# Performance work log

Measured on AMD Instinct MI355X. Metric: run time of the kernel, lower is better.

The kernel has to match this reference:

```python
import jax, jax.numpy as jnp
import numpy as np

B, T, D = 64, 2048, 512
H = 64           # hidden_size
K, S = 3, 3      # kernel_size, stride
PAD = (K - 1) // 2
BATCH_FACTOR = 0.5


def _ceil_div(a, b):
    return -(-a // b)


def _conv1d(x, w, b, stride, padding):
    # x: [B, C_in, T], w: [C_out, C_in, K] (torch Conv1d layout), b: [C_out]
    y = jax.lax.conv_general_dilated(
        x, w, window_strides=(stride,), padding=[(padding, padding)],
        dimension_numbers=("NCH", "OIH", "NCH"))
    return y + b[None, :, None]


def _score_estimator(x, seq_lens, w1, b1, w2, b2):
    # x: [B, T, D] -> scores [B, T''], seq lens [B]
    xc = jnp.transpose(x, (0, 2, 1))                     # [B, D, T]
    h = _conv1d(xc, w1, b1, S, PAD)                      # [B, 2H, T']
    h = h.reshape(h.shape[0], H, 2, h.shape[-1]).max(axis=2)  # maxout pairs -> [B, H, T']
    s = _conv1d(h, w2, b2, S, PAD)[:, 0, :]              # [B, T'']
    sl = _ceil_div(seq_lens - K + 1 + 2 * PAD, S)
    sl = _ceil_div(sl - K + 1 + 2 * PAD, S)
    return s, sl


def setup_inputs() -> dict:
    key = jax.random.key(0)
    ks = jax.random.split(key, 6)
    x = jax.random.normal(ks[0], (B, T, D), dtype=jnp.float32)
    seq_lens = jax.random.randint(ks[1], (B,), T // 2, T + 1)
    w1 = jax.random.normal(ks[2], (2 * H, D, K), dtype=jnp.float32) * (1.0 / np.sqrt(D * K))
    b1 = jax.random.normal(ks[3], (2 * H,), dtype=jnp.float32) * 0.01
    w2 = jax.random.normal(ks[4], (1, H, K), dtype=jnp.float32) * (1.0 / np.sqrt(H * K))
    b2 = jax.random.normal(ks[5], (1,), dtype=jnp.float32) * 0.01
    return {"x": x, "seq_lens": seq_lens, "w1": w1, "b1": b1, "w2": w2, "b2": b2}


def reference(x, seq_lens, w1, b1, w2, b2):
    scores, scores_sl = _score_estimator(x, seq_lens, w1, b1, w2, b2)  # [B, T''], [B]
    # mean over (padded) time, rescaled by T''/seq_len (torch true division -> float)
    est = scores.mean(axis=1) * (scores.shape[1] / scores_sl.astype(jnp.float32))  # [B]
    k = int(scores.shape[0] * BATCH_FACTOR)
    _, idx = jax.lax.top_k(est, k)
    # torch builds a boolean mask + masked_select, which preserves original batch order
    idx = jnp.sort(idx)
    sel_lens = seq_lens[idx]                              # [B']
    x_sel = x[idx]                                        # [B', T, D]
    # torch also truncates time to max(sel_lens); drops only padding frames.
    # Done eagerly here (data-dependent shape, so not inside jit).
    max_time = int(jnp.max(sel_lens))
    x_sel = x_sel[:, :max_time, :]
    return x_sel, sel_lens
```

## Files before the change

kernel.cpp:

```cpp
#include <hip/hip_runtime.h>

#define T_LEN 2048
#define D_DIM 512
#define B_SZ  64
#define T1_LEN 683
#define NSEL  32
#define KTOT  1536
#define BK    64
#define TILE_T1 96
#define NTILES 8
#define NITER (KTOT / BK)

typedef __attribute__((ext_vector_type(8))) short bf16x8;
typedef __attribute__((ext_vector_type(4))) float f32x4;

constexpr size_t OFF_WHI = 0;
constexpr size_t OFF_WLO = 393216;
constexpr size_t OFF_EST = 786432;
constexpr size_t OFF_SEL = 786944;

__device__ inline unsigned bf16_rne(float x) {
    unsigned u = __float_as_uint(x);
    return (u + 0x7FFFu + ((u >> 16) & 1u)) >> 16;
}

__device__ inline unsigned bf16_rhu(float x) {
    return (__float_as_uint(x) + 0x8000u) >> 16;
}

__global__ __launch_bounds__(256) void pack_w1_split(const float* __restrict__ w1,
                                                     unsigned short* __restrict__ whi,
                                                     unsigned short* __restrict__ wlo,
                                                     float* __restrict__ est_raw) {
    if (blockIdx.x == 0 && threadIdx.x < 64) est_raw[threadIdx.x] = 0.f;
    int idx = blockIdx.x * 256 + threadIdx.x;
    int k0blk = idx >> 13;
    int rem   = idx & 8191;
    int row   = rem >> 6;
    int col   = rem & 63;
    int c8s   = col >> 3;
    int e     = col & 7;
    int c8    = c8s ^ (row & 7);
    int kap   = (k0blk << 6) + (c8 << 3) + e;
    int k = kap >> 9, d = kap & 511;
    float v = w1[row * 1536 + d * 3 + k];
    unsigned hb = bf16_rne(v);
    float hf = __uint_as_float(hb << 16);
    whi[idx] = (unsigned short)hb;
    wlo[idx] = (unsigned short)bf16_rne(v - hf);
}

__global__ __launch_bounds__(256, 2) void conv1_mfma(
        const float* __restrict__ x,
        const unsigned short* __restrict__ whi,
        const unsigned short* __restrict__ wlo,
        const float* __restrict__ b1,
        const float* __restrict__ w2,
        float* __restrict__ est_raw) {
    __shared__ __align__(16) unsigned short Ahi[128 * 64];
    __shared__ __align__(16) unsigned short Alo[128 * 64];
    __shared__ __align__(16) unsigned short Bhi[96 * 64];
    __shared__ __align__(16) unsigned short Blo[96 * 64];
    __shared__ float b1s[128];
    __shared__ float w2s[192];
    __shared__ float red[256];

    const int tid  = threadIdx.x;
    const int lane = tid & 63;
    const int w    = tid >> 6;
    const int b    = blockIdx.y;
    const int t1g0 = blockIdx.x * TILE_T1;

    if (tid < 128) b1s[tid] = b1[tid];
    if (tid < 192) w2s[tid] = w2[tid];

    const float* xb = x + (size_t)b * (T_LEN * (size_t)D_DIM);

    const int l15  = lane & 15;
    const int quad = lane >> 4;
    const int c0w  = (w >> 1) * 64;
    const int t0w  = (w & 1) * 48;

    int offA[4], swA[4];
    #pragma unroll
    for (int mi = 0; mi < 4; ++mi) { int r = c0w + mi * 16 + l15; offA[mi] = r * 64; swA[mi] = r & 7; }
    int offB[3], swB[3];
    #pragma unroll
    for (int ni = 0; ni < 3; ++ni) { int r = t0w + ni * 16 + l15; offB[ni] = r * 64; swB[ni] = r & 7; }

    int bdst[3], gb[3], bok[3];
    #pragma unroll
    for (int q = 0; q < 3; ++q) {
        int id = tid + 256 * q;
        int row = id >> 3, c8 = id & 7;
        int t1abs = t1g0 + row;
        bok[q]  = (t1abs < T1_LEN);
        gb[q]   = 1536 * t1abs + c8 * 8 - 512;
        bdst[q] = row * 64 + ((c8 ^ (row & 7)) << 3);
    }

    f32x4 acc[4][3];
    #pragma unroll
    for (int mi = 0; mi < 4; ++mi)
        #pragma unroll
        for (int ni = 0; ni < 3; ++ni) acc[mi][ni] = (f32x4){0.f, 0.f, 0.f, 0.f};

    int4  arh[4], arl[4];
    float4 br[6];

    auto load_stage = [&](int k0) {
        const int4* ph = (const int4*)(whi) + (k0 >> 6) * 1024 + tid;
        const int4* pl = (const int4*)(wlo) + (k0 >> 6) * 1024 + tid;
        #pragma unroll
        for (int q = 0; q < 4; ++q) arh[q] = ph[q * 256];
        #pragma unroll
        for (int q = 0; q < 4; ++q) arl[q] = pl[q * 256];
        #pragma unroll
        for (int q = 0; q < 3; ++q) {
            int g = gb[q] + k0;
            float4 z = make_float4(0.f, 0.f, 0.f, 0.f);
            if (bok[q] && g >= 0) {
                br[2 * q]     = *(const float4*)(xb + g);
                br[2 * q + 1] = *(const float4*)(xb + g + 4);
            } else {
                br[2 * q] = z; br[2 * q + 1] = z;
            }
        }
    };

    auto write_stage = [&]() {
        #pragma unroll
        for (int q = 0; q < 4; ++q) ((int4*)Ahi)[tid + q * 256] = arh[q];
        #pragma unroll
        for (int q = 0; q < 4; ++q) ((int4*)Alo)[tid + q * 256] = arl[q];
        #pragma unroll
        for (int q = 0; q < 3; ++q) {
            float fv[8] = {br[2*q].x, br[2*q].y, br[2*q].z, br[2*q].w,
                           br[2*q+1].x, br[2*q+1].y, br[2*q+1].z, br[2*q+1].w};
            unsigned hp[4], lp[4];
            #pragma unroll
            for (int e = 0; e < 4; ++e) {
                unsigned h0 = bf16_rhu(fv[2 * e]);
                unsigned h1 = bf16_rhu(fv[2 * e + 1]);
                float r0 = fv[2 * e]     - __uint_as_float(h0 << 16);
                float r1 = fv[2 * e + 1] - __uint_as_float(h1 << 16);
                unsigned l0 = bf16_rhu(r0);
                unsigned l1 = bf16_rhu(r1);
                hp[e] = h0 | (h1 << 16);
                lp[e] = l0 | (l1 << 16);
            }
            *(int4*)(Bhi + bdst[q]) = make_int4(hp[0], hp[1], hp[2], hp[3]);
            *(int4*)(Blo + bdst[q]) = make_int4(lp[0], lp[1], lp[2], lp[3]);
        }
    };

    load_stage(0);
    write_stage();
    __syncthreads();

    for (int it = 0; it < NITER; ++it) {
        if (it < NITER - 1) load_stage((it + 1) * BK);

        #pragma unroll
        for (int ks = 0; ks < 2; ++ks) {
            const int ch = ks * 4 + quad;
            bf16x8 ah[4], al[4], bh[3], bl[3];
            #pragma unroll
            for (int mi = 0; mi < 4; ++mi) {
                int o = offA[mi] + ((ch ^ swA[mi]) << 3);
                ah[mi] = *(const bf16x8*)(Ahi + o);
                al[mi] = *(const bf16x8*)(Alo + o);
            }
            #pragma unroll
            for (int ni = 0; ni < 3; ++ni) {
                int o = offB[ni] + ((ch ^ swB[ni]) << 3);
                bh[ni] = *(const bf16x8*)(Bhi + o);
                bl[ni] = *(const bf16x8*)(Blo + o);
            }
            #pragma unroll
            for (int mi = 0; mi < 4; ++mi)
                #pragma unroll
                for (int ni = 0; ni < 3; ++ni) {
                    acc[mi][ni] = __builtin_amdgcn_mfma_f32_16x16x32_bf16(ah[mi], bh[ni], acc[mi][ni], 0, 0, 0);
                    acc[mi][ni] = __builtin_amdgcn_mfma_f32_16x16x32_bf16(ah[mi], bl[ni], acc[mi][ni], 0, 0, 0);
                    acc[mi][ni] = __builtin_amdgcn_mfma_f32_16x16x32_bf16(al[mi], bh[ni], acc[mi][ni], 0, 0, 0);
                }
        }
        __syncthreads();
        if (it < NITER - 1) {
            write_stage();
            __syncthreads();
        }
    }

    float contrib = 0.f;
    #pragma unroll
    for (int mi = 0; mi < 4; ++mi) {
        const int cbase = c0w + mi * 16 + (quad << 2);
        const float bb0 = b1s[cbase], bb1 = b1s[cbase + 1];
        const float bb2 = b1s[cbase + 2], bb3 = b1s[cbase + 3];
        const int j0 = cbase >> 1;
        #pragma unroll
        for (int ni = 0; ni < 3; ++ni) {
            const int t1 = t1g0 + t0w + ni * 16 + l15;
            if (t1 < T1_LEN) {
                float p0 = fmaxf(acc[mi][ni][0] + bb0, acc[mi][ni][1] + bb1);
                float p1 = fmaxf(acc[mi][ni][2] + bb2, acc[mi][ni][3] + bb3);
                int r = (t1 + 1) % 3;
                contrib += p0 * w2s[j0 * 3 + r] + p1 * w2s[(j0 + 1) * 3 + r];
            }
        }
    }
    red[tid] = contrib;
    __syncthreads();
    for (int off = 128; off > 0; off >>= 1) {
        if (tid < off) red[tid] += red[tid + off];
        __syncthreads();
    }
    if (tid == 0) atomicAdd(est_raw + b, red[0]);
}

__global__ void select_k(const float* __restrict__ est_raw,
                         const float* __restrict__ b2,
                         const int* __restrict__ seq_lens,
                         int* __restrict__ sel,
                         float* __restrict__ out_lens) {
    const int i = threadIdx.x;
    __shared__ float e[64];
    const int L  = seq_lens[i];
    const int sl = ((L + 2) / 3 + 2) / 3;
    const float ei = (est_raw[i] + 228.0f * b2[0]) / (float)sl;
    e[i] = ei;
    __syncthreads();
    int rank = 0;
    for (int j = 0; j < 64; ++j) {
        float ej = e[j];
        rank += (ej > ei) || (ej == ei && j < i);
    }
    const bool selq = rank < NSEL;
    const unsigned long long m = __ballot(selq);
    if (selq) {
        int pos = __popcll(m & ((1ull << i) - 1ull));
        sel[pos] = i;
        out_lens[pos] = (float)L;
    }
}

__global__ __launch_bounds__(256) void gather_rows(const float* __restrict__ x,
                                                   const int* __restrict__ sel,
                                                   float* __restrict__ out,
                                                   int n4row) {
    const int i = blockIdx.y;
    const int v = blockIdx.x * 256 + threadIdx.x;
    if (v < n4row) {
        const int src = sel[i];
        const float4* xs = (const float4*)(x + (size_t)src * T_LEN * D_DIM);
        float4* od = (float4*)(out + (size_t)i * ((size_t)n4row * 4));
        od[v] = xs[v];
    }
}

extern "C" void kernel_launch(void* const* d_in, const int* in_sizes, int n_in,
                              void* d_out, int out_size, void* d_ws, size_t ws_size,
                              hipStream_t stream) {
    const float* x        = (const float*)d_in[0];
    const int*   seq_lens = (const int*)  d_in[1];
    const float* w1       = (const float*)d_in[2];
    const float* b1       = (const float*)d_in[3];
    const float* w2       = (const float*)d_in[4];
    const float* b2       = (const float*)d_in[5];
    float* out = (float*)d_out;

    char* ws = (char*)d_ws;
    unsigned short* whi = (unsigned short*)(ws + OFF_WHI);
    unsigned short* wlo = (unsigned short*)(ws + OFF_WLO);
    float* est_raw = (float*)(ws + OFF_EST);
    int*   sel     = (int*)  (ws + OFF_SEL);

    const int max_time = (out_size - NSEL) / (NSEL * D_DIM);

    pack_w1_split<<<768, 256, 0, stream>>>(w1, whi, wlo, est_raw);
    conv1_mfma<<<dim3(NTILES, B_SZ), 256, 0, stream>>>(x, whi, wlo, b1, w2, est_raw);
    select_k<<<1, 64, 0, stream>>>(est_raw, b2, seq_lens, sel,
                                   out + (size_t)NSEL * max_time * D_DIM);
    const int n4row = max_time * (D_DIM / 4);
    gather_rows<<<dim3((n4row + 255) / 256, NSEL), 256, 0, stream>>>(x, sel, out, n4row);
}
```

Before: 511.0 us.

## Load weight tiles directly to LDS and use truncating bf16 split via perm

Weight hi/lo tiles are now copied straight from global memory into LDS with global_load_lds, which bypasses registers. The register-prefetch double-buffer pipeline is removed, so each iteration loads, converts and computes in sequence with two barriers. The activation bf16 hi/lo split now truncates with byte-permute instead of round-half-up. This cuts register pressure and per-element ALU work, but gives up load/compute overlap and changes rounding of the hi part (the lo residual compensates).

```diff
diff --git a/kernel.cpp b/kernel.cpp
--- a/kernel.cpp
+++ b/kernel.cpp
@@ -24,8 +24,11 @@
     return (u + 0x7FFFu + ((u >> 16) & 1u)) >> 16;
 }
 
-__device__ inline unsigned bf16_rhu(float x) {
-    return (__float_as_uint(x) + 0x8000u) >> 16;
+__device__ __forceinline__ void gload_lds16(const void* g, void* l) {
+    __builtin_amdgcn_global_load_lds(
+        (const __attribute__((address_space(1))) unsigned int*)g,
+        (__attribute__((address_space(3))) unsigned int*)l,
+        16, 0, 0);
 }
 
 __global__ __launch_bounds__(256) void pack_w1_split(const float* __restrict__ w1,
@@ -105,61 +108,58 @@
         #pragma unroll
         for (int ni = 0; ni < 3; ++ni) acc[mi][ni] = (f32x4){0.f, 0.f, 0.f, 0.f};
 
-    int4  arh[4], arl[4];
-    float4 br[6];
-
-    auto load_stage = [&](int k0) {
-        const int4* ph = (const int4*)(whi) + (k0 >> 6) * 1024 + tid;
-        const int4* pl = (const int4*)(wlo) + (k0 >> 6) * 1024 + tid;
-        #pragma unroll
-        for (int q = 0; q < 4; ++q) arh[q] = ph[q * 256];
-        #pragma unroll
-        for (int q = 0; q < 4; ++q) arl[q] = pl[q * 256];
+    for (int it = 0; it < NITER; ++it) {
+        const int k0 = it * BK;
+
+        float4 bv0 = make_float4(0.f,0.f,0.f,0.f), bv1 = bv0, bv2 = bv0,
+               bv3 = bv0, bv4 = bv0, bv5 = bv0;
+        {
+            int g0 = gb[0] + k0, g1 = gb[1] + k0, g2 = gb[2] + k0;
+            if (bok[0] && g0 >= 0) { bv0 = *(const float4*)(xb + g0); bv1 = *(const float4*)(xb + g0 + 4); }
+            if (bok[1] && g1 >= 0) { bv2 = *(const float4*)(xb + g1); bv3 = *(const float4*)(xb + g1 + 4); }
+            if (bok[2] && g2 >= 0) { bv4 = *(const float4*)(xb + g2); bv5 = *(const float4*)(xb + g2 + 4); }
+        }
+
+        {
+            const unsigned short* sH = whi + it * 8192 + tid * 8;
+            const unsigned short* sL = wlo + it * 8192 + tid * 8;
+            unsigned short* dH = Ahi + tid * 8;
+            unsigned short* dL = Alo + tid * 8;
+            #pragma unroll
+            for (int s = 0; s < 4; ++s) {
+                gload_lds16(sH + s * 2048, dH + s * 2048);
+                gload_lds16(sL + s * 2048, dL + s * 2048);
+            }
+        }
+
         #pragma unroll
         for (int q = 0; q < 3; ++q) {
-            int g = gb[q] + k0;
-            float4 z = make_float4(0.f, 0.f, 0.f, 0.f);
-            if (bok[q] && g >= 0) {
-                br[2 * q]     = *(const float4*)(xb + g);
-                br[2 * q + 1] = *(const float4*)(xb + g + 4);
-            } else {
-                br[2 * q] = z; br[2 * q + 1] = z;
-            }
-        }
-    };
-
-    auto write_stage = [&]() {
-        #pragma unroll
-        for (int q = 0; q < 4; ++q) ((int4*)Ahi)[tid + q * 256] = arh[q];
-        #pragma unroll
-        for (int q = 0; q < 4; ++q) ((int4*)Alo)[tid + q * 256] = arl[q];
-        #pragma unroll
-        for (int q = 0; q < 3; ++q) {
-            float fv[8] = {br[2*q].x, br[2*q].y, br[2*q].z, br[2*q].w,
-                           br[2*q+1].x, br[2*q+1].y, br[2*q+1].z, br[2*q+1].w};
-            unsigned hp[4], lp[4];
-            #pragma unroll
-            for (int e = 0; e < 4; ++e) {
-                unsigned h0 = bf16_rhu(fv[2 * e]);
-                unsigned h1 = bf16_rhu(fv[2 * e + 1]);
-                float r0 = fv[2 * e]     - __uint_as_float(h0 << 16);
-                float r1 = fv[2 * e + 1] - __uint_as_float(h1 << 16);
-                unsigned l0 = bf16_rhu(r0);
-                unsigned l1 = bf16_rhu(r1);
-                hp[e] = h0 | (h1 << 16);
-                lp[e] = l0 | (l1 << 16);
-            }
-            *(int4*)(Bhi + bdst[q]) = make_int4(hp[0], hp[1], hp[2], hp[3]);
-            *(int4*)(Blo + bdst[q]) = make_int4(lp[0], lp[1], lp[2], lp[3]);
-        }
-    };
-
-    load_stage(0);
-    write_stage();
-    __syncthreads();
-
-    for (int it = 0; it < NITER; ++it) {
-        if (it < NITER - 1) load_stage((it + 1) * BK);
+            float4 va = (q == 0) ? bv0 : (q == 1) ? bv2 : bv4;
+            float4 vb = (q == 0) ? bv1 : (q == 1) ? bv3 : bv5;
+            unsigned f0 = __float_as_uint(va.x), f1 = __float_as_uint(va.y);
+            unsigned f2 = __float_as_uint(va.z), f3 = __float_as_uint(va.w);
+            unsigned f4 = __float_as_uint(vb.x), f5 = __float_as_uint(vb.y);
+            unsigned f6 = __float_as_uint(vb.z), f7 = __float_as_uint(vb.w);
+            unsigned hp0 = __builtin_amdgcn_perm(f1, f0, 0x07060302u);
+            unsigned hp1 = __builtin_amdgcn_perm(f3, f2, 0x07060302u);
+            unsigned hp2 = __builtin_amdgcn_perm(f5, f4, 0x07060302u);
+            unsigned hp3 = __builtin_amdgcn_perm(f7, f6, 0x07060302u);
+            float r0 = va.x - __uint_as_float(f0 & 0xFFFF0000u);
+            float r1 = va.y - __uint_as_float(f1 & 0xFFFF0000u);
+            float r2 = va.z - __uint_as_float(f2 & 0xFFFF0000u);
+            float r3 = va.w - __uint_as_float(f3 & 0xFFFF0000u);
+            float r4 = vb.x - __uint_as_float(f4 & 0xFFFF0000u);
+            float r5 = vb.y - __uint_as_float(f5 & 0xFFFF0000u);
+            float r6 = vb.z - __uint_as_float(f6 & 0xFFFF0000u);
+            float r7 = vb.w - __uint_as_float(f7 & 0xFFFF0000u);
+            unsigned lp0 = __builtin_amdgcn_perm(__float_as_uint(r1), __float_as_uint(r0), 0x07060302u);
+            unsigned lp1 = __builtin_amdgcn_perm(__float_as_uint(r3), __float_as_uint(r2), 0x07060302u);
+            unsigned lp2 = __builtin_amdgcn_perm(__float_as_uint(r5), __float_as_uint(r4), 0x07060302u);
+            unsigned lp3 = __builtin_amdgcn_perm(__float_as_uint(r7), __float_as_uint(r6), 0x07060302u);
+            *(int4*)(Bhi + bdst[q]) = make_int4(hp0, hp1, hp2, hp3);
+            *(int4*)(Blo + bdst[q]) = make_int4(lp0, lp1, lp2, lp3);
+        }
+        __syncthreads();
 
         #pragma unroll
         for (int ks = 0; ks < 2; ++ks) {
@@ -187,10 +187,6 @@
                 }
         }
         __syncthreads();
-        if (it < NITER - 1) {
-            write_stage();
-            __syncthreads();
-        }
     }
 
     float contrib = 0.f;
```

After: 444.1 us. 13.1% less time.
